# Kernel optimization log

Measured on AMD Instinct MI355X. Metric: run time of the kernel, lower is better.

The kernel has to match this reference:

```python
import jax, jax.numpy as jnp
import numpy as np

# ---- sizes / physics constants ----
N = 16384            # batch
HID = 64             # hidden_dim
GRID = 1000          # voltage grid_size
VMIN, VMAX = -1.25, 0.0
I_TARGET = 200.0     # target current density
F_CONST = 96485.33   # Faraday constant [C/mol]
RT = 8.314 * 298.15  # gas constant * T
D_CO2 = 1.91e-9      # CO2 diffusion coefficient [m^2/s]
C_CO2 = 34.0         # CO2 saturation concentration [mol/m^3]
# equilibrium potentials for [CO, C2H4, H2b]
E_EQ = np.array([-0.11, 0.08, 0.0], dtype=np.float32)
# electrons transferred per CO2 for the CO2-consuming reactions [CO, C2H4]
N_ELEC_CO2 = np.array([2.0, 12.0], dtype=np.float32)


def _xavier(k, fan_in, fan_out):
    lim = float(np.sqrt(6.0 / (fan_in + fan_out)))
    return jax.random.uniform(k, (fan_in, fan_out), jnp.float32, -lim, lim)


def setup_inputs() -> dict:
    key = jax.random.key(0)
    ks = jax.random.split(key, 6)
    return {
        "x": jax.random.normal(ks[0], (N, 5), jnp.float32),
        "W1": _xavier(ks[1], 5, HID), "b1": jnp.zeros((HID,), jnp.float32),
        "W2": _xavier(ks[2], HID, HID), "b2": jnp.zeros((HID,), jnp.float32),
        "W3": _xavier(ks[3], HID, HID), "b3": jnp.zeros((HID,), jnp.float32),
        "W4": _xavier(ks[4], HID, 6), "b4": jnp.zeros((6,), jnp.float32),
        # learnable Butler-Volmer kinetics for [CO, C2H4, H2b]
        "i0": jnp.array([4.7e-4, 2.5e-6, 1.0e-5], jnp.float32),
        "alpha": jnp.array([0.44, 0.40, 0.36], jnp.float32),
    }


def reference(x, W1, b1, W2, b2, W3, b3, W4, b4, i0, alpha):
    # MLP (dropout inactive at inference) -> latent physical parameters
    h = jax.nn.relu(x @ W1 + b1)
    h = jax.nn.relu(h @ W2 + b2)
    h = jax.nn.relu(h @ W3 + b3)
    lat = h @ W4 + b4                              # [N, 6]

    r = 4e-8 * jnp.exp(lat[:, 0:1])                # pore radius [N,1]
    eps = jax.nn.sigmoid(lat[:, 1:2])              # porosity [N,1]
    zlt = x[:, 3:4]                                 # zlt_mu_stds = (0, 1)
    L = zlt / (1.0 - eps)                           # layer thickness [N,1]
    K_dl_factor = jnp.exp(lat[:, 2:3])              # [N,1]
    thetas = jax.nn.softmax(2.0 * lat[:, 3:6], axis=-1)  # [N,3] site fractions

    # Bruggeman effective diffusivity and GDL mass-transfer coefficient
    D_eff = D_CO2 * eps ** 1.5                      # [N,1]
    K_gdl = K_dl_factor * D_eff / r                 # [N,1]
    # series transport resistance: GDL + catalyst layer
    K_tot = 1.0 / (1.0 / K_gdl + jnp.abs(L) / D_eff)        # [N,1]
    i_lim_co2 = jnp.asarray(N_ELEC_CO2) * F_CONST * K_tot * C_CO2  # [N,2]
    # H2 evolution is not CO2-transport-limited -> zero inverse limit
    i_lim_inv = jnp.concatenate([1.0 / i_lim_co2, jnp.zeros_like(K_tot)], axis=-1)  # [N,3]

    # Butler-Volmer partial currents over the voltage grid
    V = jnp.linspace(VMIN, VMAX, GRID, dtype=jnp.float32)         # [G]
    eta = V[None, :, None] - jnp.asarray(E_EQ)                    # [1,G,3]
    i_kin = thetas[:, None, :] * i0 * jnp.exp(-alpha * (F_CONST / RT) * eta)  # [N,G,3]
    i_sp = 1.0 / (1.0 / i_kin + i_lim_inv[:, None, :])            # [N,G,3]
    i_tot = i_sp.sum(-1)                                          # [N,G]

    # grid root-finding: voltage where total current matches the target
    idx = jnp.argmin(jnp.abs(i_tot - I_TARGET), axis=1)           # [N]
    i_sel = jnp.take_along_axis(i_sp, idx[:, None, None], axis=1)[:, 0, :]  # [N,3]
    fe = i_sel / i_sel.sum(-1, keepdims=True)                     # Faradaic efficiencies

    # output = [FE_C2H4, FE_CO]
    return jnp.concatenate([fe[:, 1:2], fe[:, 0:1]], axis=-1)
```

## Files before the change

kernel.cpp:

```cpp
#include <hip/hip_runtime.h>
#include <math.h>

typedef __attribute__((ext_vector_type(4))) float f32x4;

__device__ __forceinline__ float rcpf(float x){ return __builtin_amdgcn_rcpf(x); }

__global__ __launch_bounds__(512, 2) void phys5(
    const float* __restrict__ x,
    const float* __restrict__ W1, const float* __restrict__ b1,
    const float* __restrict__ W2, const float* __restrict__ b2,
    const float* __restrict__ W3, const float* __restrict__ b3,
    const float* __restrict__ W4, const float* __restrict__ b4,
    const float* __restrict__ i0p, const float* __restrict__ alphap,
    float* __restrict__ out, int nrows)
{
    __shared__ float hb[64*64];
    __shared__ __align__(16) float tab4[4000];
    __shared__ float latb[64*8];

    const int tid  = threadIdx.x;
    const int lane = tid & 63;
    const int wvu  = __builtin_amdgcn_readfirstlane(tid >> 6);
    const int c0u  = 8*wvu;

    {
        const float KFRT = (float)(96485.33/(8.314*298.15));
        const float dV = 1.25f/999.0f;
        float a0=alphap[0], a1=alphap[1], a2=alphap[2];
        float i00=i0p[0], i01=i0p[1], i02=i0p[2];
        for (int v = tid; v < 1000; v += 512){
            float Vv = -1.25f + (float)v*dV;
            tab4[v*4+0] = expf(a0*KFRT*(Vv+0.11f))/i00;
            tab4[v*4+1] = expf(a1*KFRT*(Vv-0.08f))/i01;
            tab4[v*4+2] = expf(a2*KFRT*(Vv))/i02;
            tab4[v*4+3] = 0.f;
        }
    }

    const int rowg = blockIdx.x*64 + lane;
    const int rowc = min(rowg, nrows-1);
    float xv[5];
#pragma unroll
    for (int i=0;i<5;i++) xv[i] = x[rowc*5+i];

    float hs[8];
#pragma unroll
    for (int j=0;j<8;j++){
        int c = c0u + j;
        float hv = b1[c];
        hv = fmaf(xv[0], W1[0*64+c], hv);
        hv = fmaf(xv[1], W1[1*64+c], hv);
        hv = fmaf(xv[2], W1[2*64+c], hv);
        hv = fmaf(xv[3], W1[3*64+c], hv);
        hv = fmaf(xv[4], W1[4*64+c], hv);
        hs[j] = fmaxf(hv, 0.f);
    }

#pragma unroll
    for (int j=0;j<8;j++) hb[(c0u+j)*64 + lane] = hs[j];
    __syncthreads();

#define BIGLAYER(W, B)                                                   \
    {                                                                    \
        float A[4][8];                                                   \
        _Pragma("unroll")                                                \
        for (int j=0;j<8;j++){ A[0][j]=B[c0u+j]; A[1][j]=0.f; A[2][j]=0.f; A[3][j]=0.f; } \
        _Pragma("unroll 16")                                             \
        for (int k=0;k<64;k++){                                          \
            float hk = hb[k*64 + lane];                                  \
            _Pragma("unroll")                                            \
            for (int j=0;j<8;j++)                                        \
                A[k&3][j] = fmaf(hk, W[k*64 + c0u + j], A[k&3][j]);      \
        }                                                                \
        _Pragma("unroll")                                                \
        for (int j=0;j<8;j++)                                            \
            hs[j] = fmaxf((A[0][j]+A[1][j])+(A[2][j]+A[3][j]), 0.f);     \
    }

    BIGLAYER(W2, b2);
    __syncthreads();
#pragma unroll
    for (int j=0;j<8;j++) hb[(c0u+j)*64 + lane] = hs[j];
    __syncthreads();

    BIGLAYER(W3, b3);
    __syncthreads();
#pragma unroll
    for (int j=0;j<8;j++) hb[(c0u+j)*64 + lane] = hs[j];
    __syncthreads();

    if (wvu < 6){
        float p[64];
#pragma unroll
        for (int k=0;k<64;k++) p[k] = hb[k*64 + lane] * W4[k*6 + wvu];
#pragma unroll
        for (int off=32; off>0; off>>=1){
#pragma unroll
            for (int m=0;m<32;m++){
                if (m < off) p[m] += p[m+off];
            }
        }
        latb[lane*8+wvu] = p[0] + b4[wvu];
    }
    __syncthreads();

    const int row = tid >> 3;
    const int cg  = tid & 7;
    const int rw  = (tid >> 3) & 7;
    const int rowg2 = blockIdx.x*64 + row;
    const int rowc2 = min(rowg2, nrows-1);

    const float lat0=latb[row*8+0], lat1=latb[row*8+1], lat2=latb[row*8+2];
    const float lat3=latb[row*8+3], lat4=latb[row*8+4], lat5=latb[row*8+5];
    const float x3 = x[rowc2*5+3];

    float rr   = 4e-8f * __expf(lat0);
    float epsv = rcpf(1.0f + __expf(-lat1));
    float Kdl  = __expf(lat2);
    float Deff = 1.91e-9f * epsv * sqrtf(epsv);
    float Kgdl = Kdl * Deff * rcpf(rr);
    float S    = rcpf(Kgdl) + fabsf(x3) * rcpf((1.0f - epsv) * Deff);
    float il0  = S * (float)(1.0 / (2.0  * 96485.33 * 34.0));
    float il1  = S * (float)(1.0 / (12.0 * 96485.33 * 34.0));

    float t0s = 2.0f*lat3, t1s = 2.0f*lat4, t2s = 2.0f*lat5;
    float mx = fmaxf(t0s, fmaxf(t1s, t2s));
    float e0 = __expf(t0s-mx), e1 = __expf(t1s-mx), e2 = __expf(t2s-mx);
    float se = e0 + e1 + e2;
    float it0 = se*rcpf(e0), it1 = se*rcpf(e1), it2 = se*rcpf(e2);

    auto itot = [&](int v) -> float {
        f32x4 tb = *(const f32x4*)&tab4[v*4];
        return rcpf(fmaf(tb.x, it0, il0)) + rcpf(fmaf(tb.y, it1, il1)) + rcpf(tb.z*it2);
    };

    bool le0f = itot(0)   <= 200.0f;
    bool le9f = itot(999) <= 200.0f;

    int lo = 0, hi = 999;
#pragma unroll 1
    for (int rd = 0; rd < 3; ++rd){
        int L = hi - lo;
        int p = lo + (L*(cg+1))/9;
        bool le = itot(p) <= 200.0f;
        unsigned long long bal = __ballot(le);
        unsigned m8 = (unsigned)((bal >> (8*rw)) & 0xFFull);
        int tz  = (m8 == 0u) ? 8 : (int)__builtin_ctz(m8);
        int nlo = (tz > 0) ? lo + (L*tz)/9 : lo;
        int nhi = (tz < 8) ? lo + (L*(tz+1))/9 : hi;
        lo = nlo; hi = nhi;
    }
    {
        int mid = lo + ((hi-lo)>>1);
        bool lem = itot(mid) <= 200.0f;
        hi = lem ? mid : hi;
        lo = lem ? lo  : mid;
    }
    float da = itot(lo) - 200.0f;
    float db = 200.0f - itot(hi);
    int idx = (da <= db) ? lo : hi;
    if (!le9f) idx = 999;
    if (le0f)  idx = 0;

    f32x4 tb = *(const f32x4*)&tab4[idx*4];
    float s0 = rcpf(fmaf(tb.x, it0, il0));
    float s1 = rcpf(fmaf(tb.y, it1, il1));
    float s2 = rcpf(tb.z*it2);
    float inv = rcpf(s0 + s1 + s2);

    if (cg == 0 && rowg2 < nrows){
        float2 o; o.x = s1*inv; o.y = s0*inv;
        reinterpret_cast<float2*>(out)[rowg2] = o;
    }
}

extern "C" void kernel_launch(void* const* d_in, const int* in_sizes, int n_in,
                              void* d_out, int out_size, void* d_ws, size_t ws_size,
                              hipStream_t stream) {
    (void)n_in; (void)d_ws; (void)ws_size; (void)out_size;
    int nrows = in_sizes[0] / 5;
    int nblk = (nrows + 63) / 64;
    phys5<<<dim3(nblk), dim3(512), 0, stream>>>(
        (const float*)d_in[0],
        (const float*)d_in[1], (const float*)d_in[2],
        (const float*)d_in[3], (const float*)d_in[4],
        (const float*)d_in[5], (const float*)d_in[6],
        (const float*)d_in[7], (const float*)d_in[8],
        (const float*)d_in[9], (const float*)d_in[10],
        (float*)d_out, nrows);
}
```

Before: 14.68 us.

## Restructure MLP to 256 threads with register-held activations and per-lane bisection search

Blocks shrink from 512 to 256 threads, and each wave now computes 16 output columns. Each lane holds its row's full hidden vector in registers, read with vectorized loads from padded, double-buffered shared memory. The last layer is computed per lane, so the cross-wave latent reduction and its extra barrier go away. The shared exponential table is dropped: each row runs a 10-step scalar bisection that evaluates expf directly, replacing the cooperative 8-way ballot search. This removes table setup and several syncs, but adds transcendental work per probe and much higher register pressure (64 activations plus 16 accumulators).

```diff
diff --git a/kernel.cpp b/kernel.cpp
--- a/kernel.cpp
+++ b/kernel.cpp
@@ -5,7 +5,9 @@
 
 __device__ __forceinline__ float rcpf(float x){ return __builtin_amdgcn_rcpf(x); }
 
-__global__ __launch_bounds__(512, 2) void phys5(
+#define HS 68
+
+__global__ __launch_bounds__(256, 4) void phys8(
     const float* __restrict__ x,
     const float* __restrict__ W1, const float* __restrict__ b1,
     const float* __restrict__ W2, const float* __restrict__ b2,
@@ -14,28 +16,13 @@
     const float* __restrict__ i0p, const float* __restrict__ alphap,
     float* __restrict__ out, int nrows)
 {
-    __shared__ float hb[64*64];
-    __shared__ __align__(16) float tab4[4000];
-    __shared__ float latb[64*8];
+    __shared__ __align__(16) float hbA[64*HS];
+    __shared__ __align__(16) float hbB[64*HS];
 
     const int tid  = threadIdx.x;
     const int lane = tid & 63;
     const int wvu  = __builtin_amdgcn_readfirstlane(tid >> 6);
-    const int c0u  = 8*wvu;
-
-    {
-        const float KFRT = (float)(96485.33/(8.314*298.15));
-        const float dV = 1.25f/999.0f;
-        float a0=alphap[0], a1=alphap[1], a2=alphap[2];
-        float i00=i0p[0], i01=i0p[1], i02=i0p[2];
-        for (int v = tid; v < 1000; v += 512){
-            float Vv = -1.25f + (float)v*dV;
-            tab4[v*4+0] = expf(a0*KFRT*(Vv+0.11f))/i00;
-            tab4[v*4+1] = expf(a1*KFRT*(Vv-0.08f))/i01;
-            tab4[v*4+2] = expf(a2*KFRT*(Vv))/i02;
-            tab4[v*4+3] = 0.f;
-        }
-    }
+    const int c0   = 16*wvu;
 
     const int rowg = blockIdx.x*64 + lane;
     const int rowc = min(rowg, nrows-1);
@@ -43,10 +30,10 @@
 #pragma unroll
     for (int i=0;i<5;i++) xv[i] = x[rowc*5+i];
 
-    float hs[8];
+    float hs[16];
 #pragma unroll
-    for (int j=0;j<8;j++){
-        int c = c0u + j;
+    for (int j=0;j<16;j++){
+        int c = c0 + j;
         float hv = b1[c];
         hv = fmaf(xv[0], W1[0*64+c], hv);
         hv = fmaf(xv[1], W1[1*64+c], hv);
@@ -56,121 +43,125 @@
         hs[j] = fmaxf(hv, 0.f);
     }
 
-#pragma unroll
-    for (int j=0;j<8;j++) hb[(c0u+j)*64 + lane] = hs[j];
-    __syncthreads();
+#define PUBLISH(BUF)                                                     \
+    {                                                                    \
+        _Pragma("unroll")                                                \
+        for (int q=0;q<4;q++){                                           \
+            f32x4 t; t.x=hs[4*q]; t.y=hs[4*q+1]; t.z=hs[4*q+2]; t.w=hs[4*q+3]; \
+            *(f32x4*)&BUF[lane*HS + c0 + 4*q] = t;                       \
+        }                                                                \
+    }
+
+    float h[64];
+#define CONSUME(BUF)                                                     \
+    {                                                                    \
+        _Pragma("unroll")                                                \
+        for (int q=0;q<16;q++){                                          \
+            f32x4 t = *(const f32x4*)&BUF[lane*HS + 4*q];                \
+            h[4*q]=t.x; h[4*q+1]=t.y; h[4*q+2]=t.z; h[4*q+3]=t.w;        \
+        }                                                                \
+    }
 
 #define BIGLAYER(W, B)                                                   \
     {                                                                    \
-        float A[4][8];                                                   \
+        float acc[16];                                                   \
         _Pragma("unroll")                                                \
-        for (int j=0;j<8;j++){ A[0][j]=B[c0u+j]; A[1][j]=0.f; A[2][j]=0.f; A[3][j]=0.f; } \
-        _Pragma("unroll 16")                                             \
+        for (int j=0;j<16;j++) acc[j] = B[c0+j];                         \
+        _Pragma("unroll")                                                \
         for (int k=0;k<64;k++){                                          \
-            float hk = hb[k*64 + lane];                                  \
             _Pragma("unroll")                                            \
-            for (int j=0;j<8;j++)                                        \
-                A[k&3][j] = fmaf(hk, W[k*64 + c0u + j], A[k&3][j]);      \
+            for (int j=0;j<16;j++)                                       \
+                acc[j] = fmaf(h[k], W[k*64 + c0 + j], acc[j]);           \
         }                                                                \
         _Pragma("unroll")                                                \
-        for (int j=0;j<8;j++)                                            \
-            hs[j] = fmaxf((A[0][j]+A[1][j])+(A[2][j]+A[3][j]), 0.f);     \
+        for (int j=0;j<16;j++) hs[j] = fmaxf(acc[j], 0.f);               \
     }
 
+    PUBLISH(hbA);
+    __syncthreads();
+    CONSUME(hbA);
     BIGLAYER(W2, b2);
+    PUBLISH(hbB);
     __syncthreads();
+    CONSUME(hbB);
+    BIGLAYER(W3, b3);
+    PUBLISH(hbA);
+    __syncthreads();
+    CONSUME(hbA);
+
+    float lat[6];
 #pragma unroll
-    for (int j=0;j<8;j++) hb[(c0u+j)*64 + lane] = hs[j];
-    __syncthreads();
+    for (int c=0;c<6;c++){
+        float a = b4[c];
+#pragma unroll
+        for (int k=0;k<64;k++) a = fmaf(h[k], W4[k*6+c], a);
+        lat[c] = a;
+    }
 
-    BIGLAYER(W3, b3);
-    __syncthreads();
-#pragma unroll
-    for (int j=0;j<8;j++) hb[(c0u+j)*64 + lane] = hs[j];
-    __syncthreads();
+    const float KFRT = (float)(96485.33/(8.314*298.15));
+    const float dV   = 1.25f/999.0f;
+    const float ALP0 = alphap[0], ALP1 = alphap[1], ALP2 = alphap[2];
+    const float IO0  = i0p[0],   IO1  = i0p[1],   IO2  = i0p[2];
 
-    if (wvu < 6){
-        float p[64];
-#pragma unroll
-        for (int k=0;k<64;k++) p[k] = hb[k*64 + lane] * W4[k*6 + wvu];
-#pragma unroll
-        for (int off=32; off>0; off>>=1){
-#pragma unroll
-            for (int m=0;m<32;m++){
-                if (m < off) p[m] += p[m+off];
-            }
-        }
-        latb[lane*8+wvu] = p[0] + b4[wvu];
-    }
-    __syncthreads();
-
-    const int row = tid >> 3;
-    const int cg  = tid & 7;
-    const int rw  = (tid >> 3) & 7;
-    const int rowg2 = blockIdx.x*64 + row;
-    const int rowc2 = min(rowg2, nrows-1);
-
-    const float lat0=latb[row*8+0], lat1=latb[row*8+1], lat2=latb[row*8+2];
-    const float lat3=latb[row*8+3], lat4=latb[row*8+4], lat5=latb[row*8+5];
-    const float x3 = x[rowc2*5+3];
-
-    float rr   = 4e-8f * __expf(lat0);
-    float epsv = rcpf(1.0f + __expf(-lat1));
-    float Kdl  = __expf(lat2);
+    float rr   = 4e-8f * __expf(lat[0]);
+    float epsv = rcpf(1.0f + __expf(-lat[1]));
+    float Kdl  = __expf(lat[2]);
     float Deff = 1.91e-9f * epsv * sqrtf(epsv);
     float Kgdl = Kdl * Deff * rcpf(rr);
-    float S    = rcpf(Kgdl) + fabsf(x3) * rcpf((1.0f - epsv) * Deff);
+    float S    = rcpf(Kgdl) + fabsf(xv[3]) * rcpf((1.0f - epsv) * Deff);
     float il0  = S * (float)(1.0 / (2.0  * 96485.33 * 34.0));
     float il1  = S * (float)(1.0 / (12.0 * 96485.33 * 34.0));
 
-    float t0s = 2.0f*lat3, t1s = 2.0f*lat4, t2s = 2.0f*lat5;
+    float t0s = 2.0f*lat[3], t1s = 2.0f*lat[4], t2s = 2.0f*lat[5];
     float mx = fmaxf(t0s, fmaxf(t1s, t2s));
     float e0 = __expf(t0s-mx), e1 = __expf(t1s-mx), e2 = __expf(t2s-mx);
     float se = e0 + e1 + e2;
     float it0 = se*rcpf(e0), it1 = se*rcpf(e1), it2 = se*rcpf(e2);
 
+    float M0 = it0 / IO0, M1 = it1 / IO1, M2 = it2 / IO2;
+    float aK0 = ALP0*KFRT, aK1 = ALP1*KFRT, aK2 = ALP2*KFRT;
+
     auto itot = [&](int v) -> float {
-        f32x4 tb = *(const f32x4*)&tab4[v*4];
-        return rcpf(fmaf(tb.x, it0, il0)) + rcpf(fmaf(tb.y, it1, il1)) + rcpf(tb.z*it2);
+        float Vv = -1.25f + (float)v*dV;
+        float q0 = fmaf(expf(aK0*(Vv+0.11f)), M0, il0);
+        float q1 = fmaf(expf(aK1*(Vv-0.08f)), M1, il1);
+        float q2 = expf(aK2*Vv) * M2;
+        return rcpf(q0) + rcpf(q1) + rcpf(q2);
     };
 
-    bool le0f = itot(0)   <= 200.0f;
-    bool le9f = itot(999) <= 200.0f;
+    float f0   = itot(0);
+    float f999 = itot(999);
+    bool le0 = f0   <= 200.0f;
+    bool le9 = f999 <= 200.0f;
 
     int lo = 0, hi = 999;
+    float flo = f0, fhi = f999;
 #pragma unroll 1
-    for (int rd = 0; rd < 3; ++rd){
-        int L = hi - lo;
-        int p = lo + (L*(cg+1))/9;
-        bool le = itot(p) <= 200.0f;
-        unsigned long long bal = __ballot(le);
-        unsigned m8 = (unsigned)((bal >> (8*rw)) & 0xFFull);
-        int tz  = (m8 == 0u) ? 8 : (int)__builtin_ctz(m8);
-        int nlo = (tz > 0) ? lo + (L*tz)/9 : lo;
-        int nhi = (tz < 8) ? lo + (L*(tz+1))/9 : hi;
-        lo = nlo; hi = nhi;
+    for (int it = 0; it < 10; ++it){
+        int mid = (lo + hi) >> 1;
+        float fm = itot(mid);
+        bool le = fm <= 200.0f;
+        hi  = le ? mid : hi;
+        fhi = le ? fm  : fhi;
+        lo  = le ? lo  : mid;
+        flo = le ? flo : fm;
     }
+    float da = flo - 200.0f;
+    float db = 200.0f - fhi;
+    int idx = (da <= db) ? lo : hi;
+    if (!le9) idx = 999;
+    if (le0)  idx = 0;
+
     {
-        int mid = lo + ((hi-lo)>>1);
-        bool lem = itot(mid) <= 200.0f;
-        hi = lem ? mid : hi;
-        lo = lem ? lo  : mid;
-    }
-    float da = itot(lo) - 200.0f;
-    float db = 200.0f - itot(hi);
-    int idx = (da <= db) ? lo : hi;
-    if (!le9f) idx = 999;
-    if (le0f)  idx = 0;
-
-    f32x4 tb = *(const f32x4*)&tab4[idx*4];
-    float s0 = rcpf(fmaf(tb.x, it0, il0));
-    float s1 = rcpf(fmaf(tb.y, it1, il1));
-    float s2 = rcpf(tb.z*it2);
-    float inv = rcpf(s0 + s1 + s2);
-
-    if (cg == 0 && rowg2 < nrows){
-        float2 o; o.x = s1*inv; o.y = s0*inv;
-        reinterpret_cast<float2*>(out)[rowg2] = o;
+        float Vv = -1.25f + (float)idx*dV;
+        float s0 = rcpf(fmaf(expf(aK0*(Vv+0.11f)), M0, il0));
+        float s1 = rcpf(fmaf(expf(aK1*(Vv-0.08f)), M1, il1));
+        float s2 = rcpf(expf(aK2*Vv) * M2);
+        float inv = rcpf(s0 + s1 + s2);
+        if (rowg < nrows){
+            float2 o; o.x = s1*inv; o.y = s0*inv;
+            reinterpret_cast<float2*>(out)[rowg] = o;
+        }
     }
 }
 
@@ -180,7 +171,7 @@
     (void)n_in; (void)d_ws; (void)ws_size; (void)out_size;
     int nrows = in_sizes[0] / 5;
     int nblk = (nrows + 63) / 64;
-    phys5<<<dim3(nblk), dim3(512), 0, stream>>>(
+    phys8<<<dim3(nblk), dim3(256), 0, stream>>>(
         (const float*)d_in[0],
         (const float*)d_in[1], (const float*)d_in[2],
         (const float*)d_in[3], (const float*)d_in[4],
```

Result: slower. 22.46 us (+53.0%).
